# Kernel tuning notes

Hardware: AMD Instinct MI355X
Metric: run time of the kernel (lower is better)

## Reference

```python
import jax, jax.numpy as jnp
import numpy as np
import math

NUM_HEADS = 16
D_KV = 64
D_MODEL = 1024
NUM_BUCKETS = 32
MAX_DISTANCE = 128
SEQ = 2048
BATCH = 2


def _relative_position_bucket(relative_position):
    # bidirectional T5 bucketing
    num_buckets = NUM_BUCKETS // 2  # 16
    buckets = (relative_position > 0).astype(jnp.int32) * num_buckets
    rp = jnp.abs(relative_position)
    max_exact = num_buckets // 2  # 8
    is_small = rp < max_exact
    rp_safe = jnp.maximum(rp, 1)  # avoid log(0); masked by is_small anyway
    rp_large = max_exact + (
        jnp.log(rp_safe.astype(jnp.float32) / max_exact)
        / math.log(MAX_DISTANCE / max_exact)
        * (num_buckets - max_exact)
    ).astype(jnp.int32)
    rp_large = jnp.minimum(rp_large, num_buckets - 1)
    return buckets + jnp.where(is_small, rp, rp_large)


def _position_bias(rel_bias_table, q_len, k_len):
    ctx = jnp.arange(q_len)[:, None]
    mem = jnp.arange(k_len)[None, :]
    buckets = _relative_position_bucket(mem - ctx)  # (q,k)
    vals = rel_bias_table[buckets]  # (q,k,h)
    return jnp.transpose(vals, (2, 0, 1))[None]  # (1,h,q,k)


def setup_inputs() -> dict:
    key = jax.random.key(0)
    ks = jax.random.split(key, 6)
    s = 1.0 / math.sqrt(D_MODEL)
    return {
        "hidden_states": jax.random.normal(ks[0], (BATCH, SEQ, D_MODEL), jnp.float32),
        "Wq": jax.random.normal(ks[1], (D_MODEL, NUM_HEADS * D_KV), jnp.float32) * s,
        "Wk": jax.random.normal(ks[2], (D_MODEL, NUM_HEADS * D_KV), jnp.float32) * s,
        "Wv": jax.random.normal(ks[3], (D_MODEL, NUM_HEADS * D_KV), jnp.float32) * s,
        "Wo": jax.random.normal(ks[4], (NUM_HEADS * D_KV, D_MODEL), jnp.float32) * s,
        "rel_bias_table": jax.random.normal(ks[5], (NUM_BUCKETS, NUM_HEADS), jnp.float32),
    }


def reference(hidden_states, Wq, Wk, Wv, Wo, rel_bias_table):
    b, s, _ = hidden_states.shape
    q = (hidden_states @ Wq).reshape(b, s, NUM_HEADS, D_KV).transpose(0, 2, 1, 3)
    k = (hidden_states @ Wk).reshape(b, s, NUM_HEADS, D_KV).transpose(0, 2, 1, 3)
    v = (hidden_states @ Wv).reshape(b, s, NUM_HEADS, D_KV).transpose(0, 2, 1, 3)
    # T5: NO query scaling, additive relative-position bias
    scores = jnp.einsum("bhqd,bhkd->bhqk", q, k) + _position_bias(rel_bias_table, s, s)
    attn = jax.nn.softmax(scores, axis=-1)  # dropout is identity in eval
    out = jnp.einsum("bhqk,bhkd->bhqd", attn, v)
    out = out.transpose(0, 2, 1, 3).reshape(b, s, NUM_HEADS * D_KV)
    return out @ Wo
```

## Files before the change

kernel.cpp:

```cpp
#include <hip/hip_runtime.h>
#include <hip/hip_bf16.h>

#define NUM_HEADS 16
#define D_KV 64
#define D_MODEL 1024
#define SEQ 2048
#define BATCH 2

using bf16x8 = __attribute__((ext_vector_type(8))) short;
using bf16x4 = __attribute__((ext_vector_type(4))) short;
using f32x4  = __attribute__((ext_vector_type(4))) float;
typedef unsigned short ushort_t;

#define HAS_1K __has_builtin(__builtin_amdgcn_mfma_f32_16x16x16bf16_1k)

__device__ inline float bf2f(unsigned short u) {
  union { unsigned int i; float f; } v; v.i = ((unsigned int)u) << 16; return v.f;
}
__device__ inline unsigned short f2bf(float f) {
  union { float f; unsigned int i; } v; v.f = f;
  unsigned int u = v.i;
  return (unsigned short)((u + 0x7FFFu + ((u >> 16) & 1u)) >> 16);
}
__device__ inline unsigned short f2bf_fast(float f) {
  union { float f; unsigned int i; } v; v.f = f;
  return (unsigned short)((v.i + 0x8000u) >> 16);
}

__device__ inline void gld_lds16(const unsigned short* g, unsigned short* l) {
  __builtin_amdgcn_global_load_lds(
      (const __attribute__((address_space(1))) unsigned int*)g,
      (__attribute__((address_space(3))) unsigned int*)l, 16, 0, 0);
}

__global__ __launch_bounds__(256) void convert_f2b(const float* __restrict__ in,
                                                   unsigned short* __restrict__ out, int n) {
  int i = (blockIdx.x * 256 + threadIdx.x) * 8;
  if (i >= n) return;
  __align__(16) unsigned short tmp[8];
#pragma unroll
  for (int e = 0; e < 8; e++) tmp[e] = f2bf(in[i + e]);
  *(uint4*)&out[i] = *(uint4*)tmp;
}

__global__ __launch_bounds__(256) void transpose_f2b4(const float* __restrict__ A0,
                                                      const float* __restrict__ A1,
                                                      const float* __restrict__ A2,
                                                      const float* __restrict__ A3,
                                                      unsigned short* __restrict__ out) {
  __shared__ __align__(16) unsigned short T[64][72];
  const float* in = (blockIdx.z == 0) ? A0 : (blockIdx.z == 1) ? A1 : (blockIdx.z == 2) ? A2 : A3;
  unsigned short* o = out + (long)blockIdx.z * 1048576;
  int r0 = blockIdx.x * 64, c0 = blockIdx.y * 64;
  int t = threadIdx.x;
#pragma unroll
  for (int i = 0; i < 2; i++) {
    int c = t + 256 * i; int r = c >> 3, k8 = (c & 7) * 8;
    const float* src = &in[(long)(r0 + r) * 1024 + c0 + k8];
    __align__(16) unsigned short tmp[8];
#pragma unroll
    for (int e = 0; e < 8; e++) tmp[e] = f2bf(src[e]);
    *(uint4*)&T[r][k8] = *(uint4*)tmp;
  }
  __syncthreads();
#pragma unroll
  for (int i = 0; i < 2; i++) {
    int c = t + 256 * i; int r = c >> 3, k8 = (c & 7) * 8;
    __align__(16) unsigned short tmp[8];
#pragma unroll
    for (int e = 0; e < 8; e++) tmp[e] = T[k8 + e][r];
    *(uint4*)&o[(long)(c0 + r) * 1024 + r0 + k8] = *(uint4*)tmp;
  }
}

__global__ __launch_bounds__(256) void transpose_b2b(const unsigned short* __restrict__ in,
                                                     unsigned short* __restrict__ out,
                                                     int in_stride, int out_stride,
                                                     long in_bstride, long out_bstride) {
  __shared__ __align__(16) unsigned short T[64][72];
  in  += blockIdx.z * in_bstride;
  out += blockIdx.z * out_bstride;
  int r0 = blockIdx.x * 64, c0 = blockIdx.y * 64;
  int t = threadIdx.x;
#pragma unroll
  for (int i = 0; i < 2; i++) {
    int c = t + 256 * i; int r = c >> 3, k8 = (c & 7) * 8;
    *(uint4*)&T[r][k8] = *(const uint4*)&in[(long)(r0 + r) * in_stride + c0 + k8];
  }
  __syncthreads();
#pragma unroll
  for (int i = 0; i < 2; i++) {
    int c = t + 256 * i; int r = c >> 3, k8 = (c & 7) * 8;
    __align__(16) unsigned short tmp[8];
#pragma unroll
    for (int e = 0; e < 8; e++) tmp[e] = T[k8 + e][r];
    *(uint4*)&out[(long)(c0 + r) * out_stride + r0 + k8] = *(uint4*)tmp;
  }
}

__global__ void bias_kernel(const float* __restrict__ tbl, unsigned short* __restrict__ biasB) {
  int idx = blockIdx.x * 64 + threadIdx.x;
  if (idx >= 4095) return;
  int rel = idx - 2047;
  int bucket = (rel > 0) ? 16 : 0;
  int rp = rel < 0 ? -rel : rel;
  int add;
  if (rp < 8) add = rp;
  else {
    int rl = 8 + (int)(logf((float)rp * 0.125f) / logf(16.0f) * 8.0f);
    add = rl < 15 ? rl : 15;
  }
  bucket += add;
#pragma unroll
  for (int h = 0; h < 16; h++) biasB[h * 4095 + idx] = f2bf(tbl[bucket * 16 + h]);
}

__global__ __launch_bounds__(256) void gemm_kernel(const unsigned short* __restrict__ X,
                                                   const unsigned short* __restrict__ Wt,
                                                   unsigned short* __restrict__ out_b,
                                                   float* __restrict__ out_f, int mode) {
  __shared__ __align__(16) unsigned short As[128 * 32];
  __shared__ __align__(16) unsigned short Bs[128 * 32];
  const int K = 1024;
  int m0 = blockIdx.x * 128;
  int n0 = blockIdx.y * 128;
  const unsigned short* W = Wt + (long)blockIdx.z * 1048576;
  unsigned short* outq = (mode == 0) ? out_b + (long)blockIdx.z * 4194304 : nullptr;
  int t = threadIdx.x;
  int w = t >> 6, l = t & 63;
  int wr = (w >> 1) * 64, wc = (w & 1) * 64;
  int lr = l & 15, lq = l >> 4;
  f32x4 acc[4][4];
#pragma unroll
  for (int i = 0; i < 4; i++)
#pragma unroll
    for (int j = 0; j < 4; j++) acc[i][j] = (f32x4){0.f, 0.f, 0.f, 0.f};

  for (int k0 = 0; k0 < K; k0 += 32) {
#pragma unroll
    for (int i = 0; i < 2; i++) {
      int c = t + 256 * i;
      int r = c >> 2, kc = (c & 3) * 8;
      gld_lds16(&X[(long)(m0 + r) * K + k0 + kc], &As[c * 8]);
      gld_lds16(&W[(long)(n0 + r) * K + k0 + kc], &Bs[c * 8]);
    }
    __syncthreads();
    bf16x8 a[4], b[4];
#pragma unroll
    for (int mi = 0; mi < 4; mi++) a[mi] = *(const bf16x8*)&As[(wr + mi * 16 + lr) * 32 + lq * 8];
#pragma unroll
    for (int ni = 0; ni < 4; ni++) b[ni] = *(const bf16x8*)&Bs[(wc + ni * 16 + lr) * 32 + lq * 8];
#pragma unroll
    for (int mi = 0; mi < 4; mi++)
#pragma unroll
      for (int ni = 0; ni < 4; ni++)
        acc[mi][ni] = __builtin_amdgcn_mfma_f32_16x16x32_bf16(a[mi], b[ni], acc[mi][ni], 0, 0, 0);
    __syncthreads();
  }
#pragma unroll
  for (int mi = 0; mi < 4; mi++)
#pragma unroll
    for (int ni = 0; ni < 4; ni++)
#pragma unroll
      for (int r = 0; r < 4; r++) {
        int m = m0 + wr + mi * 16 + lq * 4 + r;
        int n = n0 + wc + ni * 16 + lr;
        float vf = acc[mi][ni][r];
        if (mode == 0) {
          int b_ = m >> 11, s = m & 2047, h = n >> 6, d = n & 63;
          outq[(((long)(b_ * NUM_HEADS + h) * SEQ) + s) * 64 + d] = f2bf(vf);
        } else {
          out_f[(long)m * 1024 + n] = vf;
        }
      }
}

#if HAS_1K
#define NBUF 2
#else
#define NBUF 1
#endif
__global__ __launch_bounds__(256, 2) void attn_kernel(const unsigned short* __restrict__ Q,
                                                      const unsigned short* __restrict__ Km,
                                                      const unsigned short* __restrict__ Vt,
                                                      const unsigned short* __restrict__ biasB,
                                                      unsigned short* __restrict__ O) {
  __shared__ __align__(16) unsigned short Ks[NBUF][64 * 72];
  __shared__ __align__(16) unsigned short Vs[NBUF][64 * 72];
  __shared__ __align__(16) unsigned short biasR[4][2176];
#if !HAS_1K
  __shared__ __align__(16) unsigned short PsQ[128 * 72];
#endif
  int q0 = blockIdx.x * 128;
  int bh = blockIdx.y;
  int b_ = bh >> 4, h = bh & 15;
  const unsigned short* Qb = Q  + (long)bh * SEQ * 64;
  const unsigned short* Kb = Km + (long)bh * SEQ * 64;
  const unsigned short* Vb = Vt + (long)bh * 64 * SEQ;
  const unsigned short* btab = biasB + h * 4095;
  int t = threadIdx.x;
  int w = t >> 6, l = t & 63;
  int lr = l & 15, lq = l >> 4;
  int qw = w * 32;

  int gbase = 1920 - q0;
  for (int i = t; i < 2176; i += 256) {
#pragma unroll
    for (int j = 0; j < 4; j++) {
      int gi = i + j; if (gi > 2174) gi = 2174;
      biasR[j][i] = btab[gbase + gi];
    }
  }

  bf16x8 aq[2][2];
#pragma unroll
  for (int qt = 0; qt < 2; qt++)
#pragma unroll
    for (int ks = 0; ks < 2; ks++)
      aq[qt][ks] = *(const bf16x8*)&Qb[(long)(q0 + qw + qt * 16 + lr) * 64 + ks * 32 + lq * 8];

  int c0 = t, c1 = t + 256;
  int r0s = c0 >> 3, f0 = (c0 & 7) * 8;
  int r1s = c1 >> 3, f1 = (c1 & 7) * 8;

  uint4 kca = *(const uint4*)&Kb[(long)r0s * 64 + f0];
  uint4 kcb = *(const uint4*)&Kb[(long)r1s * 64 + f1];
  uint4 vca = *(const uint4*)&Vb[(long)r0s * SEQ + f0];
  uint4 vcb = *(const uint4*)&Vb[(long)r1s * SEQ + f1];
#if HAS_1K
  *(uint4*)&Ks[0][r0s * 72 + f0] = kca;
  *(uint4*)&Ks[0][r1s * 72 + f1] = kcb;
  *(uint4*)&Vs[0][r0s * 72 + f0] = vca;
  *(uint4*)&Vs[0][r1s * 72 + f1] = vcb;
#endif

  f32x4 accO[4][2];
  f32x4 accL[2];
#pragma unroll
  for (int qt = 0; qt < 2; qt++) {
    accL[qt] = (f32x4){0.f, 0.f, 0.f, 0.f};
#pragma unroll
    for (int dt = 0; dt < 4; dt++) accO[dt][qt] = (f32x4){0.f, 0.f, 0.f, 0.f};
  }

#if HAS_1K
  bf16x4 ones4;
#pragma unroll
  for (int e = 0; e < 4; e++) ones4[e] = (short)0x3F80;
#else
  bf16x8 ones8;
#pragma unroll
  for (int e = 0; e < 8; e++) ones8[e] = (short)0x3F80;
#endif

  int vb = 127 + lq * 4 - qw - lr;
  int bj = (3 - (lr & 3)) & 3;

  for (int k0 = 0; k0 < SEQ; k0 += 64) {
    int buf = (k0 >> 6) & (NBUF - 1);
    bool more = (k0 + 64) < SEQ;
#if HAS_1K
    if (more) {
      const unsigned short* Kn = Kb + (long)(k0 + 64) * 64;
      const unsigned short* Vn = Vb + (k0 + 64);
      kca = *(const uint4*)&Kn[(long)r0s * 64 + f0];
      kcb = *(const uint4*)&Kn[(long)r1s * 64 + f1];
      vca = *(const uint4*)&Vn[(long)r0s * SEQ + f0];
      vcb = *(const uint4*)&Vn[(long)r1s * SEQ + f1];
    }
    __syncthreads();
#else
    __syncthreads();
    *(uint4*)&Ks[0][r0s * 72 + f0] = kca;
    *(uint4*)&Ks[0][r1s * 72 + f1] = kcb;
    *(uint4*)&Vs[0][r0s * 72 + f0] = vca;
    *(uint4*)&Vs[0][r1s * 72 + f1] = vcb;
    __syncthreads();
    if (more) {
      const unsigned short* Kn = Kb + (long)(k0 + 64) * 64;
      const unsigned short* Vn = Vb + (k0 + 64);
      kca = *(const uint4*)&Kn[(long)r0s * 64 + f0];
      kcb = *(const uint4*)&Kn[(long)r1s * 64 + f1];
      vca = *(const uint4*)&Vn[(long)r0s * SEQ + f0];
      vcb = *(const uint4*)&Vn[(long)r1s * SEQ + f1];
    }
#endif

    bf16x8 bk[4][2];
#pragma unroll
    for (int kt = 0; kt < 4; kt++)
#pragma unroll
      for (int ks = 0; ks < 2; ks++)
        bk[kt][ks] = *(const bf16x8*)&Ks[buf][(kt * 16 + lr) * 72 + ks * 32 + lq * 8];

    f32x4 sacc[4][2];
#pragma unroll
    for (int kt = 0; kt < 4; kt++)
#pragma unroll
      for (int qt = 0; qt < 2; qt++) sacc[kt][qt] = (f32x4){0.f, 0.f, 0.f, 0.f};
#pragma unroll
    for (int ks = 0; ks < 2; ks++)
#pragma unroll
      for (int kt = 0; kt < 4; kt++)
#pragma unroll
        for (int qt = 0; qt < 2; qt++)
          sacc[kt][qt] = __builtin_amdgcn_mfma_f32_16x16x32_bf16(bk[kt][ks], aq[qt][ks], sacc[kt][qt], 0, 0, 0);

#if HAS_1K
    bf16x4 pk[4][2];
#endif
#pragma unroll
    for (int kt = 0; kt < 4; kt++)
#pragma unroll
      for (int qt = 0; qt < 2; qt++) {
        int base = vb + k0 + kt * 16 - qt * 16;
        uint2 braw = *(const uint2*)&biasR[bj][base - bj];
        float p0 = __expf(sacc[kt][qt][0] + bf2f((unsigned short)(braw.x & 0xffffu)));
        float p1 = __expf(sacc[kt][qt][1] + bf2f((unsigned short)(braw.x >> 16)));
        float p2 = __expf(sacc[kt][qt][2] + bf2f((unsigned short)(braw.y & 0xffffu)));
        float p3 = __expf(sacc[kt][qt][3] + bf2f((unsigned short)(braw.y >> 16)));
#if HAS_1K
        pk[kt][qt] = (bf16x4){(short)f2bf_fast(p0), (short)f2bf_fast(p1),
                              (short)f2bf_fast(p2), (short)f2bf_fast(p3)};
#else
        unsigned int d0 = ((unsigned int)f2bf_fast(p1) << 16) | f2bf_fast(p0);
        unsigned int d1 = ((unsigned int)f2bf_fast(p3) << 16) | f2bf_fast(p2);
        *(uint2*)&PsQ[(qw + qt * 16 + lr) * 72 + kt * 16 + lq * 4] = (uint2){d0, d1};
#endif
      }

#if HAS_1K
#pragma unroll
    for (int kt = 0; kt < 4; kt++) {
      bf16x4 va[4];
#pragma unroll
      for (int dt = 0; dt < 4; dt++)
        va[dt] = *(const bf16x4*)&Vs[buf][(dt * 16 + lr) * 72 + kt * 16 + lq * 4];
#pragma unroll
      for (int qt = 0; qt < 2; qt++) {
#pragma unroll
        for (int dt = 0; dt < 4; dt++)
          accO[dt][qt] = __builtin_amdgcn_mfma_f32_16x16x16bf16_1k(va[dt], pk[kt][qt], accO[dt][qt], 0, 0, 0);
        accL[qt] = __builtin_amdgcn_mfma_f32_16x16x16bf16_1k(ones4, pk[kt][qt], accL[qt], 0, 0, 0);
      }
    }
    if (more) {
      int nb = 1 - buf;
      *(uint4*)&Ks[nb][r0s * 72 + f0] = kca;
      *(uint4*)&Ks[nb][r1s * 72 + f1] = kcb;
      *(uint4*)&Vs[nb][r0s * 72 + f0] = vca;
      *(uint4*)&Vs[nb][r1s * 72 + f1] = vcb;
    }
#else
    bf16x8 bp[2][2];
#pragma unroll
    for (int ks = 0; ks < 2; ks++)
#pragma unroll
      for (int qt = 0; qt < 2; qt++)
        bp[ks][qt] = *(const bf16x8*)&PsQ[(qw + qt * 16 + lr) * 72 + ks * 32 + lq * 8];
#pragma unroll
    for (int ks = 0; ks < 2; ks++) {
      bf16x8 va8[4];
#pragma unroll
      for (int dt = 0; dt < 4; dt++)
        va8[dt] = *(const bf16x8*)&Vs[0][(dt * 16 + lr) * 72 + ks * 32 + lq * 8];
#pragma unroll
      for (int qt = 0; qt < 2; qt++) {
#pragma unroll
        for (int dt = 0; dt < 4; dt++)
          accO[dt][qt] = __builtin_amdgcn_mfma_f32_16x16x32_bf16(va8[dt], bp[ks][qt], accO[dt][qt], 0, 0, 0);
        accL[qt] = __builtin_amdgcn_mfma_f32_16x16x32_bf16(ones8, bp[ks][qt], accL[qt], 0, 0, 0);
      }
    }
#endif
  }

#pragma unroll
  for (int qt = 0; qt < 2; qt++) {
    float rl = 1.0f / accL[qt][0];
    int q = q0 + qw + qt * 16 + lr;
#pragma unroll
    for (int dt = 0; dt < 4; dt++) {
      unsigned int s0 = ((unsigned int)f2bf(accO[dt][qt][1] * rl) << 16) | f2bf(accO[dt][qt][0] * rl);
      unsigned int s1 = ((unsigned int)f2bf(accO[dt][qt][3] * rl) << 16) | f2bf(accO[dt][qt][2] * rl);
      *(uint2*)&O[((long)(b_ * SEQ + q)) * 1024 + h * 64 + dt * 16 + lq * 4] = (uint2){s0, s1};
    }
  }
}

extern "C" void kernel_launch(void* const* d_in, const int* in_sizes, int n_in,
                              void* d_out, int out_size, void* d_ws, size_t ws_size,
                              hipStream_t stream) {
  const float* X   = (const float*)d_in[0];
  const float* Wq  = (const float*)d_in[1];
  const float* Wk  = (const float*)d_in[2];
  const float* Wv  = (const float*)d_in[3];
  const float* Wo  = (const float*)d_in[4];
  const float* tbl = (const float*)d_in[5];

  unsigned short* wt    = (unsigned short*)d_ws;
  unsigned short* xbf   = wt + 4 * 1048576;
  unsigned short* q_ws  = xbf + 4194304;
  unsigned short* k_ws  = q_ws + 4194304;
  unsigned short* v_ws  = k_ws + 4194304;
  unsigned short* vt_ws = v_ws + 4194304;
  unsigned short* o_ws  = vt_ws + 4194304;
  unsigned short* biasB = o_ws + 4194304;

  convert_f2b<<<2048, 256, 0, stream>>>(X, xbf, 4194304);
  transpose_f2b4<<<dim3(16, 16, 4), 256, 0, stream>>>(Wq, Wk, Wv, Wo, wt);
  bias_kernel<<<64, 64, 0, stream>>>(tbl, biasB);
  gemm_kernel<<<dim3(32, 8, 3), 256, 0, stream>>>(xbf, wt, q_ws, nullptr, 0);
  transpose_b2b<<<dim3(32, 1, 32), 256, 0, stream>>>(v_ws, vt_ws, 64, 2048, 131072L, 131072L);
  attn_kernel<<<dim3(16, 32), 256, 0, stream>>>(q_ws, k_ws, vt_ws, biasB, o_ws);
  gemm_kernel<<<dim3(32, 8, 1), 256, 0, stream>>>(o_ws, wt + 3 * 1048576, nullptr, (float*)d_out, 1);
}
```

Before: 226.7 us.

## Fuse prep kernels, use exp2 with log2e-prescaled Q and fp32 bias, raise attention occupancy

```diff
diff --git a/kernel.cpp b/kernel.cpp
--- a/kernel.cpp
+++ b/kernel.cpp
@@ -1,22 +1,18 @@
 #include <hip/hip_runtime.h>
 #include <hip/hip_bf16.h>
+#include <math.h>
 
 #define NUM_HEADS 16
 #define D_KV 64
 #define D_MODEL 1024
 #define SEQ 2048
 #define BATCH 2
+#define LOG2E 1.4426950408889634f
 
 using bf16x8 = __attribute__((ext_vector_type(8))) short;
 using bf16x4 = __attribute__((ext_vector_type(4))) short;
 using f32x4  = __attribute__((ext_vector_type(4))) float;
-typedef unsigned short ushort_t;
-
-#define HAS_1K __has_builtin(__builtin_amdgcn_mfma_f32_16x16x16bf16_1k)
-
-__device__ inline float bf2f(unsigned short u) {
-  union { unsigned int i; float f; } v; v.i = ((unsigned int)u) << 16; return v.f;
-}
+
 __device__ inline unsigned short f2bf(float f) {
   union { float f; unsigned int i; } v; v.f = f;
   unsigned int u = v.i;
@@ -27,49 +23,88 @@
   return (unsigned short)((v.i + 0x8000u) >> 16);
 }
 
+#if __has_builtin(__builtin_amdgcn_exp2f)
+#define EXP2(x) __builtin_amdgcn_exp2f(x)
+#else
+#define EXP2(x) __expf((x) * 0.6931471805599453f)
+#endif
+
+__device__ inline unsigned int pk_bf16(float a, float b) {
+#if __has_builtin(__builtin_amdgcn_cvt_pk_bf16_f32)
+  auto v = __builtin_amdgcn_cvt_pk_bf16_f32(a, b);
+  unsigned int u; __builtin_memcpy(&u, &v, 4);
+  return u;
+#else
+  return ((unsigned int)f2bf_fast(b) << 16) | f2bf_fast(a);
+#endif
+}
+
 __device__ inline void gld_lds16(const unsigned short* g, unsigned short* l) {
   __builtin_amdgcn_global_load_lds(
       (const __attribute__((address_space(1))) unsigned int*)g,
       (__attribute__((address_space(3))) unsigned int*)l, 16, 0, 0);
 }
 
-__global__ __launch_bounds__(256) void convert_f2b(const float* __restrict__ in,
-                                                   unsigned short* __restrict__ out, int n) {
-  int i = (blockIdx.x * 256 + threadIdx.x) * 8;
-  if (i >= n) return;
-  __align__(16) unsigned short tmp[8];
-#pragma unroll
-  for (int e = 0; e < 8; e++) tmp[e] = f2bf(in[i + e]);
-  *(uint4*)&out[i] = *(uint4*)tmp;
-}
-
-__global__ __launch_bounds__(256) void transpose_f2b4(const float* __restrict__ A0,
-                                                      const float* __restrict__ A1,
-                                                      const float* __restrict__ A2,
-                                                      const float* __restrict__ A3,
-                                                      unsigned short* __restrict__ out) {
+__global__ __launch_bounds__(256) void prep_kernel(const float* __restrict__ X,
+                                                   const float* __restrict__ W0,
+                                                   const float* __restrict__ W1,
+                                                   const float* __restrict__ W2,
+                                                   const float* __restrict__ W3,
+                                                   const float* __restrict__ tbl,
+                                                   unsigned short* __restrict__ xbf,
+                                                   unsigned short* __restrict__ wt,
+                                                   float* __restrict__ biasF) {
   __shared__ __align__(16) unsigned short T[64][72];
-  const float* in = (blockIdx.z == 0) ? A0 : (blockIdx.z == 1) ? A1 : (blockIdx.z == 2) ? A2 : A3;
-  unsigned short* o = out + (long)blockIdx.z * 1048576;
-  int r0 = blockIdx.x * 64, c0 = blockIdx.y * 64;
+  int bid = blockIdx.x;
   int t = threadIdx.x;
-#pragma unroll
-  for (int i = 0; i < 2; i++) {
-    int c = t + 256 * i; int r = c >> 3, k8 = (c & 7) * 8;
-    const float* src = &in[(long)(r0 + r) * 1024 + c0 + k8];
+  if (bid < 2048) {
+    int i = (bid * 256 + t) * 8;
     __align__(16) unsigned short tmp[8];
 #pragma unroll
-    for (int e = 0; e < 8; e++) tmp[e] = f2bf(src[e]);
-    *(uint4*)&T[r][k8] = *(uint4*)tmp;
-  }
-  __syncthreads();
-#pragma unroll
-  for (int i = 0; i < 2; i++) {
-    int c = t + 256 * i; int r = c >> 3, k8 = (c & 7) * 8;
-    __align__(16) unsigned short tmp[8];
-#pragma unroll
-    for (int e = 0; e < 8; e++) tmp[e] = T[k8 + e][r];
-    *(uint4*)&o[(long)(c0 + r) * 1024 + r0 + k8] = *(uint4*)tmp;
+    for (int e = 0; e < 8; e++) tmp[e] = f2bf(X[i + e]);
+    *(uint4*)&xbf[i] = *(uint4*)tmp;
+  } else if (bid < 3072) {
+    int rem = bid - 2048;
+    int z = rem >> 8, tid = rem & 255;
+    const float* in = (z == 0) ? W0 : (z == 1) ? W1 : (z == 2) ? W2 : W3;
+    unsigned short* o = wt + (long)z * 1048576;
+    int r0 = (tid & 15) * 64, c0 = (tid >> 4) * 64;
+#pragma unroll
+    for (int i = 0; i < 2; i++) {
+      int c = t + 256 * i; int r = c >> 3, k8 = (c & 7) * 8;
+      const float* src = &in[(long)(r0 + r) * 1024 + c0 + k8];
+      __align__(16) unsigned short tmp[8];
+#pragma unroll
+      for (int e = 0; e < 8; e++) tmp[e] = f2bf(src[e]);
+      *(uint4*)&T[r][k8] = *(uint4*)tmp;
+    }
+    __syncthreads();
+#pragma unroll
+    for (int i = 0; i < 2; i++) {
+      int c = t + 256 * i; int r = c >> 3, k8 = (c & 7) * 8;
+      __align__(16) unsigned short tmp[8];
+#pragma unroll
+      for (int e = 0; e < 8; e++) tmp[e] = T[k8 + e][r];
+      *(uint4*)&o[(long)(c0 + r) * 1024 + r0 + k8] = *(uint4*)tmp;
+    }
+  } else {
+#pragma unroll
+    for (int ii = 0; ii < 16; ii++) {
+      int idx = t + 256 * ii;
+      if (idx >= 4095) break;
+      int rel = idx - 2047;
+      int bucket = (rel > 0) ? 16 : 0;
+      int rp = rel < 0 ? -rel : rel;
+      int add;
+      if (rp < 8) add = rp;
+      else {
+        int rl = 8 + (int)(logf((float)rp * 0.125f) / logf(16.0f) * 8.0f);
+        add = rl < 15 ? rl : 15;
+      }
+      bucket += add;
+#pragma unroll
+      for (int h = 0; h < 16; h++) biasF[h * 4096 + idx] = tbl[bucket * 16 + h] * LOG2E;
+    }
   }
 }
 
@@ -96,23 +131,6 @@
     for (int e = 0; e < 8; e++) tmp[e] = T[k8 + e][r];
     *(uint4*)&out[(long)(c0 + r) * out_stride + r0 + k8] = *(uint4*)tmp;
   }
-}
-
-__global__ void bias_kernel(const float* __restrict__ tbl, unsigned short* __restrict__ biasB) {
-  int idx = blockIdx.x * 64 + threadIdx.x;
-  if (idx >= 4095) return;
-  int rel = idx - 2047;
-  int bucket = (rel > 0) ? 16 : 0;
-  int rp = rel < 0 ? -rel : rel;
-  int add;
-  if (rp < 8) add = rp;
-  else {
-    int rl = 8 + (int)(logf((float)rp * 0.125f) / logf(16.0f) * 8.0f);
-    add = rl < 15 ? rl : 15;
-  }
-  bucket += add;
-#pragma unroll
-  for (int h = 0; h < 16; h++) biasB[h * 4095 + idx] = f2bf(tbl[bucket * 16 + h]);
 }
 
 __global__ __launch_bounds__(256) void gemm_kernel(const unsigned short* __restrict__ X,
@@ -126,6 +144,7 @@
   int n0 = blockIdx.y * 128;
   const unsigned short* W = Wt + (long)blockIdx.z * 1048576;
   unsigned short* outq = (mode == 0) ? out_b + (long)blockIdx.z * 4194304 : nullptr;
+  float scale = (mode == 0 && blockIdx.z == 0) ? LOG2E : 1.0f;
   int t = threadIdx.x;
   int w = t >> 6, l = t & 63;
   int wr = (w >> 1) * 64, wc = (w & 1) * 64;
@@ -165,7 +184,7 @@
       for (int r = 0; r < 4; r++) {
         int m = m0 + wr + mi * 16 + lq * 4 + r;
         int n = n0 + wc + ni * 16 + lr;
-        float vf = acc[mi][ni][r];
+        float vf = acc[mi][ni][r] * scale;
         if (mode == 0) {
           int b_ = m >> 11, s = m & 2047, h = n >> 6, d = n & 63;
           outq[(((long)(b_ * NUM_HEADS + h) * SEQ) + s) * 64 + d] = f2bf(vf);
@@ -175,29 +194,21 @@
       }
 }
 
-#if HAS_1K
-#define NBUF 2
-#else
-#define NBUF 1
-#endif
-__global__ __launch_bounds__(256, 2) void attn_kernel(const unsigned short* __restrict__ Q,
+__global__ __launch_bounds__(256, 4) void attn_kernel(const unsigned short* __restrict__ Q,
                                                       const unsigned short* __restrict__ Km,
                                                       const unsigned short* __restrict__ Vt,
-                                                      const unsigned short* __restrict__ biasB,
+                                                      const float* __restrict__ biasF,
                                                       unsigned short* __restrict__ O) {
-  __shared__ __align__(16) unsigned short Ks[NBUF][64 * 72];
-  __shared__ __align__(16) unsigned short Vs[NBUF][64 * 72];
-  __shared__ __align__(16) unsigned short biasR[4][2176];
-#if !HAS_1K
-  __shared__ __align__(16) unsigned short PsQ[128 * 72];
-#endif
+  __shared__ __align__(16) unsigned short Ks[64 * 72];
+  __shared__ __align__(16) unsigned short Vs[64 * 72];
+  __shared__ __align__(16) float biasRf[2][2176];
   int q0 = blockIdx.x * 128;
   int bh = blockIdx.y;
   int b_ = bh >> 4, h = bh & 15;
   const unsigned short* Qb = Q  + (long)bh * SEQ * 64;
   const unsigned short* Kb = Km + (long)bh * SEQ * 64;
   const unsigned short* Vb = Vt + (long)bh * 64 * SEQ;
-  const unsigned short* btab = biasB + h * 4095;
+  const float* btabF = biasF + h * 4096;
   int t = threadIdx.x;
   int w = t >> 6, l = t & 63;
   int lr = l & 15, lq = l >> 4;
@@ -205,11 +216,10 @@
 
   int gbase = 1920 - q0;
   for (int i = t; i < 2176; i += 256) {
-#pragma unroll
-    for (int j = 0; j < 4; j++) {
-      int gi = i + j; if (gi > 2174) gi = 2174;
-      biasR[j][i] = btab[gbase + gi];
-    }
+    int g0 = gbase + i;     if (g0 > 4094) g0 = 4094;
+    int g1 = gbase + i + 1; if (g1 > 4094) g1 = 4094;
+    biasRf[0][i] = btabF[g0];
+    biasRf[1][i] = btabF[g1];
   }
 
   bf16x8 aq[2][2];
@@ -227,12 +237,10 @@
   uint4 kcb = *(const uint4*)&Kb[(long)r1s * 64 + f1];
   uint4 vca = *(const uint4*)&Vb[(long)r0s * SEQ + f0];
   uint4 vcb = *(const uint4*)&Vb[(long)r1s * SEQ + f1];
-#if HAS_1K
-  *(uint4*)&Ks[0][r0s * 72 + f0] = kca;
-  *(uint4*)&Ks[0][r1s * 72 + f1] = kcb;
-  *(uint4*)&Vs[0][r0s * 72 + f0] = vca;
-  *(uint4*)&Vs[0][r1s * 72 + f1] = vcb;
-#endif
+  *(uint4*)&Ks[r0s * 72 + f0] = kca;
+  *(uint4*)&Ks[r1s * 72 + f1] = kcb;
+  *(uint4*)&Vs[r0s * 72 + f0] = vca;
+  *(uint4*)&Vs[r1s * 72 + f1] = vcb;
 
   f32x4 accO[4][2];
   f32x4 accL[2];
@@ -243,23 +251,34 @@
     for (int dt = 0; dt < 4; dt++) accO[dt][qt] = (f32x4){0.f, 0.f, 0.f, 0.f};
   }
 
-#if HAS_1K
   bf16x4 ones4;
 #pragma unroll
   for (int e = 0; e < 4; e++) ones4[e] = (short)0x3F80;
-#else
-  bf16x8 ones8;
-#pragma unroll
-  for (int e = 0; e < 8; e++) ones8[e] = (short)0x3F80;
-#endif
 
   int vb = 127 + lq * 4 - qw - lr;
-  int bj = (3 - (lr & 3)) & 3;
+  int bj2 = vb & 1;
+  const float* brow = biasRf[bj2];
+  int pbc = vb - bj2 - 16;
 
   for (int k0 = 0; k0 < SEQ; k0 += 64) {
-    int buf = (k0 >> 6) & (NBUF - 1);
+    __syncthreads();
     bool more = (k0 + 64) < SEQ;
-#if HAS_1K
+
+    float2 bbl[5][2];
+    int pb = pbc + k0;
+#pragma unroll
+    for (int m = 0; m < 5; m++) {
+      bbl[m][0] = *(const float2*)&brow[pb + 16 * m];
+      bbl[m][1] = *(const float2*)&brow[pb + 16 * m + 2];
+    }
+
+    bf16x8 bk[4][2];
+#pragma unroll
+    for (int kt = 0; kt < 4; kt++)
+#pragma unroll
+      for (int ks = 0; ks < 2; ks++)
+        bk[kt][ks] = *(const bf16x8*)&Ks[(kt * 16 + lr) * 72 + ks * 32 + lq * 8];
+
     if (more) {
       const unsigned short* Kn = Kb + (long)(k0 + 64) * 64;
       const unsigned short* Vn = Vb + (k0 + 64);
@@ -268,30 +287,6 @@
       vca = *(const uint4*)&Vn[(long)r0s * SEQ + f0];
       vcb = *(const uint4*)&Vn[(long)r1s * SEQ + f1];
     }
-    __syncthreads();
-#else
-    __syncthreads();
-    *(uint4*)&Ks[0][r0s * 72 + f0] = kca;
-    *(uint4*)&Ks[0][r1s * 72 + f1] = kcb;
-    *(uint4*)&Vs[0][r0s * 72 + f0] = vca;
-    *(uint4*)&Vs[0][r1s * 72 + f1] = vcb;
-    __syncthreads();
-    if (more) {
-      const unsigned short* Kn = Kb + (long)(k0 + 64) * 64;
-      const unsigned short* Vn = Vb + (k0 + 64);
-      kca = *(const uint4*)&Kn[(long)r0s * 64 + f0];
-      kcb = *(const uint4*)&Kn[(long)r1s * 64 + f1];
-      vca = *(const uint4*)&Vn[(long)r0s * SEQ + f0];
-      vcb = *(const uint4*)&Vn[(long)r1s * SEQ + f1];
-    }
-#endif
-
-    bf16x8 bk[4][2];
-#pragma unroll
-    for (int kt = 0; kt < 4; kt++)
-#pragma unroll
-      for (int ks = 0; ks < 2; ks++)
-        bk[kt][ks] = *(const bf16x8*)&Ks[buf][(kt * 16 + lr) * 72 + ks * 32 + lq * 8];
 
     f32x4 sacc[4][2];
 #pragma unroll
@@ -306,36 +301,27 @@
         for (int qt = 0; qt < 2; qt++)
           sacc[kt][qt] = __builtin_amdgcn_mfma_f32_16x16x32_bf16(bk[kt][ks], aq[qt][ks], sacc[kt][qt], 0, 0, 0);
 
-#if HAS_1K
     bf16x4 pk[4][2];
-#endif
 #pragma unroll
     for (int kt = 0; kt < 4; kt++)
 #pragma unroll
       for (int qt = 0; qt < 2; qt++) {
-        int base = vb + k0 + kt * 16 - qt * 16;
-        uint2 braw = *(const uint2*)&biasR[bj][base - bj];
-        float p0 = __expf(sacc[kt][qt][0] + bf2f((unsigned short)(braw.x & 0xffffu)));
-        float p1 = __expf(sacc[kt][qt][1] + bf2f((unsigned short)(braw.x >> 16)));
-        float p2 = __expf(sacc[kt][qt][2] + bf2f((unsigned short)(braw.y & 0xffffu)));
-        float p3 = __expf(sacc[kt][qt][3] + bf2f((unsigned short)(braw.y >> 16)));
-#if HAS_1K
-        pk[kt][qt] = (bf16x4){(short)f2bf_fast(p0), (short)f2bf_fast(p1),
-                              (short)f2bf_fast(p2), (short)f2bf_fast(p3)};
-#else
-        unsigned int d0 = ((unsigned int)f2bf_fast(p1) << 16) | f2bf_fast(p0);
-        unsigned int d1 = ((unsigned int)f2bf_fast(p3) << 16) | f2bf_fast(p2);
-        *(uint2*)&PsQ[(qw + qt * 16 + lr) * 72 + kt * 16 + lq * 4] = (uint2){d0, d1};
-#endif
+        int blk = kt - qt + 1;
+        float p0 = EXP2(sacc[kt][qt][0] + bbl[blk][0].x);
+        float p1 = EXP2(sacc[kt][qt][1] + bbl[blk][0].y);
+        float p2 = EXP2(sacc[kt][qt][2] + bbl[blk][1].x);
+        float p3 = EXP2(sacc[kt][qt][3] + bbl[blk][1].y);
+        unsigned int uu[2] = { pk_bf16(p0, p1), pk_bf16(p2, p3) };
+        bf16x4 pv; __builtin_memcpy(&pv, uu, 8);
+        pk[kt][qt] = pv;
       }
 
-#if HAS_1K
 #pragma unroll
     for (int kt = 0; kt < 4; kt++) {
       bf16x4 va[4];
 #pragma unroll
       for (int dt = 0; dt < 4; dt++)
-        va[dt] = *(const bf16x4*)&Vs[buf][(dt * 16 + lr) * 72 + kt * 16 + lq * 4];
+        va[dt] = *(const bf16x4*)&Vs[(dt * 16 + lr) * 72 + kt * 16 + lq * 4];
 #pragma unroll
       for (int qt = 0; qt < 2; qt++) {
 #pragma unroll
@@ -344,35 +330,14 @@
         accL[qt] = __builtin_amdgcn_mfma_f32_16x16x16bf16_1k(ones4, pk[kt][qt], accL[qt], 0, 0, 0);
       }
     }
+
+    __syncthreads();
     if (more) {
-      int nb = 1 - buf;
-      *(uint4*)&Ks[nb][r0s * 72 + f0] = kca;
-      *(uint4*)&Ks[nb][r1s * 72 + f1] = kcb;
-      *(uint4*)&Vs[nb][r0s * 72 + f0] = vca;
-      *(uint4*)&Vs[nb][r1s * 72 + f1] = vcb;
-    }
-#else
-    bf16x8 bp[2][2];
-#pragma unroll
-    for (int ks = 0; ks < 2; ks++)
-#pragma unroll
-      for (int qt = 0; qt < 2; qt++)
-        bp[ks][qt] = *(const bf16x8*)&PsQ[(qw + qt * 16 + lr) * 72 + ks * 32 + lq * 8];
-#pragma unroll
-    for (int ks = 0; ks < 2; ks++) {
-      bf16x8 va8[4];
-#pragma unroll
-      for (int dt = 0; dt < 4; dt++)
-        va8[dt] = *(const bf16x8*)&Vs[0][(dt * 16 + lr) * 72 + ks * 32 + lq * 8];
-#pragma unroll
-      for (int qt = 0; qt < 2; qt++) {
-#pragma unroll
-        for (int dt = 0; dt < 4; dt++)
-          accO[dt][qt] = __builtin_amdgcn_mfma_f32_16x16x32_bf16(va8[dt], bp[ks][qt], accO[dt][qt], 0, 0, 0);
-        accL[qt] = __builtin_amdgcn_mfma_f32_16x16x32_bf16(ones8, bp[ks][qt], accL[qt], 0, 0, 0);
-      }
-    }
-#endif
+      *(uint4*)&Ks[r0s * 72 + f0] = kca;
+      *(uint4*)&Ks[r1s * 72 + f1] = kcb;
+      *(uint4*)&Vs[r0s * 72 + f0] = vca;
+      *(uint4*)&Vs[r1s * 72 + f1] = vcb;
+    }
   }
 
 #pragma unroll
@@ -405,13 +370,11 @@
   unsigned short* v_ws  = k_ws + 4194304;
   unsigned short* vt_ws = v_ws + 4194304;
   unsigned short* o_ws  = vt_ws + 4194304;
-  unsigned short* biasB = o_ws + 4194304;
-
-  convert_f2b<<<2048, 256, 0, stream>>>(X, xbf, 4194304);
-  transpose_f2b4<<<dim3(16, 16, 4), 256, 0, stream>>>(Wq, Wk, Wv, Wo, wt);
-  bias_kernel<<<64, 64, 0, stream>>>(tbl, biasB);
+  float* biasF = (float*)(o_ws + 4194304);
+
+  prep_kernel<<<3073, 256, 0, stream>>>(X, Wq, Wk, Wv, Wo, tbl, xbf, wt, biasF);
   gemm_kernel<<<dim3(32, 8, 3), 256, 0, stream>>>(xbf, wt, q_ws, nullptr, 0);
   transpose_b2b<<<dim3(32, 1, 32), 256, 0, stream>>>(v_ws, vt_ws, 64, 2048, 131072L, 131072L);
-  attn_kernel<<<dim3(16, 32), 256, 0, stream>>>(q_ws, k_ws, vt_ws, biasB, o_ws);
+  attn_kernel<<<dim3(16, 32), 256, 0, stream>>>(q_ws, k_ws, vt_ws, biasF, o_ws);
   gemm_kernel<<<dim3(32, 8, 1), 256, 0, stream>>>(o_ws, wt + 3 * 1048576, nullptr, (float*)d_out, 1);
 }
```

After: 338.7 us. 49.4% more time.
